# Optimization experiments

Hardware: AMD Instinct MI355X
Metric: run time of the kernel (lower is better)

## Reference

```python
import jax, jax.numpy as jnp
from jax import lax
import numpy as np


def conv2d(x, w, b, stride=1, pad=0):
    # x: [B,C,H,W], w: [O,I,kh,kw]
    y = lax.conv_general_dilated(
        x, w, (stride, stride), [(pad, pad), (pad, pad)],
        dimension_numbers=("NCHW", "OIHW", "NCHW"))
    return y + b[None, :, None, None]


def setup_inputs() -> dict:
    key = jax.random.key(0)
    ks = jax.random.split(key, 9)
    B, C, Ci, H, W = 1, 64, 32, 96, 96
    sc3 = 1.0 / np.sqrt(C * 9)   # fan-in scale for 3x3 convs
    sc1 = 1.0 / np.sqrt(C)       # fan-in scale for 1x1 convs
    scw = 1.0 / np.sqrt(Ci)
    return {
        "x":    jax.random.normal(ks[0], (B, C, H, W), jnp.float32),
        "d1_w": jax.random.normal(ks[1], (C, C, 3, 3), jnp.float32) * sc3,
        "d1_b": jnp.zeros((C,), jnp.float32),
        "d2_w": jax.random.normal(ks[2], (C, C, 3, 3), jnp.float32) * sc3,
        "d2_b": jnp.zeros((C,), jnp.float32),
        "d3_w": jax.random.normal(ks[3], (C, C, 3, 3), jnp.float32) * sc3,
        "d3_b": jnp.zeros((C,), jnp.float32),
        "g_w":  jax.random.normal(ks[4], (Ci, C, 1, 1), jnp.float32) * sc1,
        "g_b":  jnp.zeros((Ci,), jnp.float32),
        "th_w": jax.random.normal(ks[5], (Ci, C, 1, 1), jnp.float32) * sc1,
        "th_b": jnp.zeros((Ci,), jnp.float32),
        "ph_w": jax.random.normal(ks[6], (Ci, C, 1, 1), jnp.float32) * sc1,
        "ph_b": jnp.zeros((Ci,), jnp.float32),
        "W_w":  jax.random.normal(ks[7], (C, Ci, 1, 1), jnp.float32) * scw,
        "W_b":  jnp.zeros((C,), jnp.float32),
    }


def reference(x, d1_w, d1_b, d2_w, d2_b, d3_w, d3_b,
              g_w, g_b, th_w, th_b, ph_w, ph_b, W_w, W_b):
    lrelu = lambda v: jnp.where(v >= 0, v, 0.2 * v)
    y = lrelu(conv2d(x, d1_w, d1_b, stride=2, pad=1))
    y = lrelu(conv2d(y, d2_w, d2_b, stride=2, pad=1))
    y = conv2d(y, d3_w, d3_b, stride=2, pad=1)
    y = jax.image.resize(y, x.shape, method="bilinear")  # align_corners=False semantics
    x = jax.nn.sigmoid(y) * x
    # --- non-local block ---
    B, C, H, W = x.shape
    Ci = g_w.shape[0]
    gx = conv2d(x, g_w, g_b).reshape(B, Ci, -1)    # [B,Ci,N]
    tx = conv2d(x, th_w, th_b).reshape(B, Ci, -1)  # [B,Ci,N]
    px = conv2d(x, ph_w, ph_b).reshape(B, Ci, -1)  # [B,Ci,N]
    # f[b,n,m] = sum_c theta[b,n,c] * phi[b,c,m]  (N x N scores, no scaling)
    f = jnp.einsum("bcn,bcm->bnm", tx, px)
    f = jax.nn.softmax(f, axis=1)  # unconventional: softmax over FIRST token axis
    # y[b,c,n] = sum_m f[b,n,m] * g[b,c,m]
    y2 = jnp.einsum("bnm,bcm->bcn", f, gx).reshape(B, Ci, H, W)
    return conv2d(y2, W_w, W_b) + x
```

## Files before the change

### kernel.cpp

```cpp
#include <hip/hip_runtime.h>
#include <math.h>

#define NTOK 9216
#define CIN  32
#define CC   64
#define NCH1 24
#define NT1S 24
#define NCH2 16
#define MS2  18
#define MCH2 576
#define LOG2E 1.4426950408889634f
#define C1INIT (-17.312340490667560f)
#define C2INIT (-9.3123404906675595f)

typedef _Float16 half8 __attribute__((ext_vector_type(8)));
typedef _Float16 half4v __attribute__((ext_vector_type(4)));
typedef float    f32x4 __attribute__((ext_vector_type(4)));

static __device__ __forceinline__ float fexp2(float x) {
#if __has_builtin(__builtin_amdgcn_exp2f)
    return __builtin_amdgcn_exp2f(x);
#else
    return exp2f(x);
#endif
}

__global__ __launch_bounds__(192) void conv3x3_lds96(const float* __restrict__ in,
                                                     const float* __restrict__ w,
                                                     float* __restrict__ outp) {
    __shared__ float li[4][3][100];
    __shared__ float lw[4][9][64];
    const int t = threadIdx.x;
    const int oh = blockIdx.x, grp = blockIdx.y;
    const int ci0 = grp * 4;
    for (int idx = t; idx < 4 * 3 * 97; idx += 192) {
        int ci = idx / (3 * 97), rem = idx % (3 * 97);
        int kh = rem / 97, col = rem % 97;
        int ih = 2 * oh - 1 + kh, iw = col - 1;
        float v = 0.f;
        if (ih >= 0 && iw >= 0) v = in[(ci0 + ci) * 9216 + ih * 96 + iw];
        li[ci][kh][col] = v;
    }
    for (int idx = t; idx < 4 * 9 * 64; idx += 192) {
        int oc = idx / 36, r = idx % 36;
        int ci = r / 9, k = r % 9;
        lw[ci][k][oc] = w[oc * 576 + (ci0 + ci) * 9 + k];
    }
    __syncthreads();
    const int oc0 = (t & 15) * 4;
    const int ow0 = (t >> 4) * 4;
    float acc[4][4] = {};
    #pragma unroll
    for (int ci = 0; ci < 4; ++ci) {
        float wr[9][4];
        #pragma unroll
        for (int k = 0; k < 9; ++k)
            *(float4*)wr[k] = *(const float4*)&lw[ci][k][oc0];
        #pragma unroll
        for (int kh = 0; kh < 3; ++kh) {
            float v[9];
            #pragma unroll
            for (int j = 0; j < 9; ++j) v[j] = li[ci][kh][2 * ow0 + j];
            #pragma unroll
            for (int px = 0; px < 4; ++px)
                #pragma unroll
                for (int kw = 0; kw < 3; ++kw) {
                    float xv = v[2 * px + kw];
                    #pragma unroll
                    for (int o = 0; o < 4; ++o)
                        acc[px][o] = fmaf(xv, wr[kh * 3 + kw][o], acc[px][o]);
                }
        }
    }
    float* op = outp + grp * (CC * 2304) + oh * 48 + ow0;
    #pragma unroll
    for (int o = 0; o < 4; ++o)
        *(float4*)(op + (oc0 + o) * 2304) =
            make_float4(acc[0][o], acc[1][o], acc[2][o], acc[3][o]);
}

template<int HIN, int HOUT, int CIG>
__global__ void conv3x3_part(const float* __restrict__ in, const float* __restrict__ w,
                             float* __restrict__ outp) {
    const int p = blockIdx.x * blockDim.x + threadIdx.x;
    if (p >= HOUT * HOUT) return;
    const int oc = blockIdx.y, grp = blockIdx.z;
    const int oh = p / HOUT, ow = p % HOUT;
    const int ci0 = grp * CIG;
    float acc = 0.f;
    #pragma unroll
    for (int ci = 0; ci < CIG; ++ci) {
        const float* ip = in + (ci0 + ci) * HIN * HIN;
        const float* wp = w + oc * CC * 9 + (ci0 + ci) * 9;
        #pragma unroll
        for (int kh = 0; kh < 3; ++kh) {
            int ih = oh * 2 - 1 + kh;
            bool okh = (unsigned)ih < (unsigned)HIN;
            #pragma unroll
            for (int kw = 0; kw < 3; ++kw) {
                int iw = ow * 2 - 1 + kw;
                float v = (okh && (unsigned)iw < (unsigned)HIN) ? ip[ih * HIN + iw] : 0.f;
                acc = fmaf(v, wp[kh * 3 + kw], acc);
            }
        }
    }
    outp[grp * (CC * HOUT * HOUT) + oc * HOUT * HOUT + p] = acc;
}

template<int NG, int HW, int LRELU>
__global__ void conv_merge4(const float* __restrict__ parts, const float* __restrict__ b,
                            float* __restrict__ out) {
    int i4 = blockIdx.x * 256 + threadIdx.x;
    int oc = (i4 * 4) / HW;
    float bb = b[oc];
    float4 acc = make_float4(bb, bb, bb, bb);
    #pragma unroll
    for (int g = 0; g < NG; ++g) {
        float4 p = *(const float4*)(parts + g * (CC * HW) + i4 * 4);
        acc.x += p.x; acc.y += p.y; acc.z += p.z; acc.w += p.w;
    }
    if (LRELU) {
        acc.x = acc.x >= 0.f ? acc.x : 0.2f * acc.x;
        acc.y = acc.y >= 0.f ? acc.y : 0.2f * acc.y;
        acc.z = acc.z >= 0.f ? acc.z : 0.2f * acc.z;
        acc.w = acc.w >= 0.f ? acc.w : 0.2f * acc.w;
    }
    *(float4*)(out + i4 * 4) = acc;
}

static __device__ __forceinline__ float gate_val(const float* y3c, int n) {
    int h = n / 96, wc = n % 96;
    float fh = (h + 0.5f) * 0.125f - 0.5f;
    float fw = (wc + 0.5f) * 0.125f - 0.5f;
    int h0 = (int)floorf(fh); float ah = fh - (float)h0;
    int w0 = (int)floorf(fw); float aw = fw - (float)w0;
    int h0c = min(max(h0, 0), 11), h1c = min(max(h0 + 1, 0), 11);
    int w0c = min(max(w0, 0), 11), w1c = min(max(w0 + 1, 0), 11);
    float v = (1.f - ah) * ((1.f - aw) * y3c[h0c * 12 + w0c] + aw * y3c[h0c * 12 + w1c])
            +         ah * ((1.f - aw) * y3c[h1c * 12 + w0c] + aw * y3c[h1c * 12 + w1c]);
    return 1.f / (1.f + __expf(-v));
}

__global__ void gate_fused(const float* __restrict__ x, const float* __restrict__ cp3,
                           const float* __restrict__ d3b, float* __restrict__ xg) {
    __shared__ float y3c[144];
    const int b = blockIdx.x, t = threadIdx.x;
    const int c = b / 36;
    if (t < 144) {
        float acc = d3b[c];
        #pragma unroll
        for (int g = 0; g < 16; ++g)
            acc += cp3[g * (CC * 144) + c * 144 + t];
        y3c[t] = acc;
    }
    __syncthreads();
    int idx = b * 256 + t;
    int n = idx % 9216;
    float sg = gate_val(y3c, n);
    xg[idx] = sg * x[idx];
}

__global__ void conv1x1_frag(const float* __restrict__ xg,
                             const float* __restrict__ gw, const float* __restrict__ gb,
                             const float* __restrict__ thw, const float* __restrict__ thb,
                             const float* __restrict__ phw, const float* __restrict__ phb,
                             _Float16* __restrict__ txF, _Float16* __restrict__ pxF,
                             _Float16* __restrict__ gxF) {
    int ci = blockIdx.y;
    int n = blockIdx.x * 256 + threadIdx.x;
    float ag = gb[ci], at = thb[ci], ap = phb[ci];
    #pragma unroll 8
    for (int c = 0; c < CC; ++c) {
        float v = xg[c * NTOK + n];
        ag = fmaf(gw[ci * CC + c],  v, ag);
        at = fmaf(thw[ci * CC + c], v, at);
        ap = fmaf(phw[ci * CC + c], v, ap);
    }
    int addr_ab = (n >> 4) * 512 + (((n & 15) | (((ci & 15) >> 2) << 4)) * 8)
                + (((ci >> 4) << 2) | (ci & 3));
    txF[addr_ab] = (_Float16)(at * LOG2E);
    pxF[addr_ab] = (_Float16)ap;
    int addr_g = ((n >> 5) * 2 + (ci >> 4)) * 512
               + (((ci & 15) | (((n & 15) >> 2) << 4)) * 8)
               + ((((n >> 4) & 1) << 2) | (n & 3));
    gxF[addr_g] = (_Float16)ag;
}

__global__ __launch_bounds__(256) void phase1(const _Float16* __restrict__ txF,
                                              const _Float16* __restrict__ pxF,
                                              float* __restrict__ Dp) {
    int w = threadIdx.x >> 6, l = threadIdx.x & 63;
    int mtile0 = (blockIdx.x * 4 + w) * 4;
    half8 pf[4];
    #pragma unroll
    for (int j = 0; j < 4; ++j)
        pf[j] = *(const half8*)(pxF + (mtile0 + j) * 512 + l * 8);
    f32x4 cini = {C1INIT, C1INIT, C1INIT, C1INIT};
    float dsum[4][4] = {};
    int nt0 = blockIdx.y * NT1S;
    #pragma unroll 2
    for (int i = 0; i < NT1S; ++i) {
        half8 tf = *(const half8*)(txF + (nt0 + i) * 512 + l * 8);
        #pragma unroll
        for (int j = 0; j < 4; ++j) {
            f32x4 s = __builtin_amdgcn_mfma_f32_16x16x32_f16(pf[j], tf, cini, 0, 0, 0);
            #pragma unroll
            for (int r = 0; r < 4; ++r)
                dsum[j][r] += fexp2(s[r]);
        }
    }
    #pragma unroll
    for (int off = 1; off < 16; off <<= 1)
        #pragma unroll
        for (int j = 0; j < 4; ++j)
            #pragma unroll
            for (int r = 0; r < 4; ++r)
                dsum[j][r] += __shfl_xor(dsum[j][r], off);
    if ((l & 15) == 0) {
        #pragma unroll
        for (int j = 0; j < 4; ++j) {
            int m = (mtile0 + j) * 16 + (l >> 4) * 4;
            #pragma unroll
            for (int r = 0; r < 4; ++r)
                Dp[blockIdx.y * NTOK + m + r] = dsum[j][r];
        }
    }
}

__global__ __launch_bounds__(256) void phase2(const _Float16* __restrict__ txF,
                                              const _Float16* __restrict__ pxF,
                                              const _Float16* __restrict__ gxF,
                                              const float* __restrict__ Dp,
                                              _Float16* __restrict__ y2p) {
    __shared__ float l2D[MCH2];
    int mbase = blockIdx.y * MCH2;
    for (int i = threadIdx.x; i < MCH2; i += 256) {
        float D = 0.f;
        #pragma unroll
        for (int ch = 0; ch < NCH1; ++ch) D += Dp[ch * NTOK + mbase + i];
        l2D[i] = __log2f(D);
    }
    __syncthreads();
    int w = threadIdx.x >> 6, l = threadIdx.x & 63;
    int ntile0 = (blockIdx.x * 4 + w) * 4;
    half8 tf[4];
    #pragma unroll
    for (int j = 0; j < 4; ++j)
        tf[j] = *(const half8*)(txF + (ntile0 + j) * 512 + l * 8);
    int khi = (l >> 4) * 4;
    f32x4 zero = {0.f, 0.f, 0.f, 0.f};
    f32x4 c2v = {C2INIT, C2INIT, C2INIT, C2INIT};
    f32x4 acc[4][2];
    #pragma unroll
    for (int j = 0; j < 4; ++j) { acc[j][0] = zero; acc[j][1] = zero; }
    #pragma unroll 2
    for (int ms = 0; ms < MS2; ++ms) {
        int m0 = mbase + ms * 32;
        int mloc = ms * 32;
        int mt16 = m0 >> 4;
        half8 pf0 = *(const half8*)(pxF + mt16 * 512 + l * 8);
        half8 pf1 = *(const half8*)(pxF + (mt16 + 1) * 512 + l * 8);
        f32x4 l2a = *(const f32x4*)&l2D[mloc + khi];
        f32x4 l2b = *(const f32x4*)&l2D[mloc + 16 + khi];
        f32x4 cini0 = c2v - l2a;
        f32x4 cini1 = c2v - l2b;
        int gt = (m0 >> 5) * 2;
        half8 gf0 = *(const half8*)(gxF + gt * 512 + l * 8);
        half8 gf1 = *(const half8*)(gxF + (gt + 1) * 512 + l * 8);
        #pragma unroll
        for (int j = 0; j < 4; ++j) {
            f32x4 s0 = __builtin_amdgcn_mfma_f32_16x16x32_f16(pf0, tf[j], cini0, 0, 0, 0);
            f32x4 s1 = __builtin_amdgcn_mfma_f32_16x16x32_f16(pf1, tf[j], cini1, 0, 0, 0);
            half8 ff;
            #pragma unroll
            for (int r = 0; r < 4; ++r) {
                ff[r]     = (_Float16)fexp2(s0[r]);
                ff[4 + r] = (_Float16)fexp2(s1[r]);
            }
            acc[j][0] = __builtin_amdgcn_mfma_f32_16x16x32_f16(ff, gf0, acc[j][0], 0, 0, 0);
            acc[j][1] = __builtin_amdgcn_mfma_f32_16x16x32_f16(ff, gf1, acc[j][1], 0, 0, 0);
        }
    }
    _Float16* base = y2p + blockIdx.y * (CIN * NTOK);
    #pragma unroll
    for (int j = 0; j < 4; ++j) {
        int n = (ntile0 + j) * 16 + khi;
        half4v v0, v1;
        #pragma unroll
        for (int r = 0; r < 4; ++r) {
            v0[r] = (_Float16)(acc[j][0][r] * 0.00390625f);
            v1[r] = (_Float16)(acc[j][1][r] * 0.00390625f);
        }
        *(half4v*)(base + (l & 15) * NTOK + n)        = v0;
        *(half4v*)(base + (16 + (l & 15)) * NTOK + n) = v1;
    }
}

__global__ void mergeY2(const _Float16* __restrict__ y2p, float* __restrict__ att) {
    int i4 = blockIdx.x * 256 + threadIdx.x;
    float4 s = make_float4(0.f, 0.f, 0.f, 0.f);
    #pragma unroll
    for (int ch = 0; ch < NCH2; ++ch) {
        half4v p = *(const half4v*)(y2p + ch * (CIN * NTOK) + i4 * 4);
        s.x += (float)p[0]; s.y += (float)p[1]; s.z += (float)p[2]; s.w += (float)p[3];
    }
    *(float4*)(att + i4 * 4) = s;
}

__global__ void final_conv(const float* __restrict__ att, const float* __restrict__ Ww,
                           const float* __restrict__ Wb, const float* __restrict__ xg,
                           float* __restrict__ out) {
    int co = blockIdx.y;
    int n = blockIdx.x * 256 + threadIdx.x;
    float acc = Wb[co];
    #pragma unroll
    for (int ci = 0; ci < CIN; ++ci)
        acc = fmaf(Ww[co * CIN + ci], att[ci * NTOK + n], acc);
    out[co * NTOK + n] = acc + xg[co * NTOK + n];
}

extern "C" void kernel_launch(void* const* d_in, const int* in_sizes, int n_in,
                              void* d_out, int out_size, void* d_ws, size_t ws_size,
                              hipStream_t stream) {
    const float* x   = (const float*)d_in[0];
    const float* d1w = (const float*)d_in[1];  const float* d1b = (const float*)d_in[2];
    const float* d2w = (const float*)d_in[3];  const float* d2b = (const float*)d_in[4];
    const float* d3w = (const float*)d_in[5];  const float* d3b = (const float*)d_in[6];
    const float* gw  = (const float*)d_in[7];  const float* gb  = (const float*)d_in[8];
    const float* thw = (const float*)d_in[9];  const float* thb = (const float*)d_in[10];
    const float* phw = (const float*)d_in[11]; const float* phb = (const float*)d_in[12];
    const float* Ww  = (const float*)d_in[13]; const float* Wb  = (const float*)d_in[14];
    float* out = (float*)d_out;

    float* W    = (float*)d_ws;
    float* xg   = W;
    float* y1   = W + 589824;
    float* y2c  = W + 737280;
    float* Dp   = W + 774144;
    float* att  = W + 995328;
    float* cp1  = W + 1290240;
    float* cp2  = W + 3649536;
    float* cp3  = W + 4239360;
    _Float16* txF  = (_Float16*)(W + 4386816);
    _Float16* pxF  = (_Float16*)(W + 4534272);
    _Float16* gxF  = (_Float16*)(W + 4681728);
    _Float16* y2pH = (_Float16*)(W + 4829184);

    conv3x3_lds96<<<dim3(48, 16), 192, 0, stream>>>(x, d1w, cp1);
    conv_merge4<16, 2304, 1><<<144, 256, 0, stream>>>(cp1, d1b, y1);
    conv3x3_part<48, 24, 4><<<dim3(3, CC, 16), 192, 0, stream>>>(y1, d2w, cp2);
    conv_merge4<16, 576, 1><<<36, 256, 0, stream>>>(cp2, d2b, y2c);
    conv3x3_part<24, 12, 4><<<dim3(1, CC, 16), 192, 0, stream>>>(y2c, d3w, cp3);
    gate_fused<<<2304, 256, 0, stream>>>(x, cp3, d3b, xg);

    conv1x1_frag<<<dim3(36, CIN), 256, 0, stream>>>(xg, gw, gb, thw, thb, phw, phb,
                                                    txF, pxF, gxF);

    phase1<<<dim3(36, NCH1), 256, 0, stream>>>(txF, pxF, Dp);
    phase2<<<dim3(36, NCH2), 256, 0, stream>>>(txF, pxF, gxF, Dp, y2pH);
    mergeY2<<<288, 256, 0, stream>>>(y2pH, att);

    final_conv<<<dim3(36, CC), 256, 0, stream>>>(att, Ww, Wb, xg, out);
}
```

Baseline: 105.9 us.

## Stage shared operands in LDS across attention and conv kernels, widen conv1 channel groups

```diff
diff --git a/kernel.cpp b/kernel.cpp
--- a/kernel.cpp
+++ b/kernel.cpp
@@ -28,21 +28,21 @@
 __global__ __launch_bounds__(192) void conv3x3_lds96(const float* __restrict__ in,
                                                      const float* __restrict__ w,
                                                      float* __restrict__ outp) {
-    __shared__ float li[4][3][100];
-    __shared__ float lw[4][9][64];
+    __shared__ float li[8][3][100];
+    __shared__ float lw[8][9][64];
     const int t = threadIdx.x;
     const int oh = blockIdx.x, grp = blockIdx.y;
-    const int ci0 = grp * 4;
-    for (int idx = t; idx < 4 * 3 * 97; idx += 192) {
-        int ci = idx / (3 * 97), rem = idx % (3 * 97);
+    const int ci0 = grp * 8;
+    for (int idx = t; idx < 8 * 3 * 97; idx += 192) {
+        int ci = idx / 291, rem = idx % 291;
         int kh = rem / 97, col = rem % 97;
         int ih = 2 * oh - 1 + kh, iw = col - 1;
         float v = 0.f;
         if (ih >= 0 && iw >= 0) v = in[(ci0 + ci) * 9216 + ih * 96 + iw];
         li[ci][kh][col] = v;
     }
-    for (int idx = t; idx < 4 * 9 * 64; idx += 192) {
-        int oc = idx / 36, r = idx % 36;
+    for (int idx = t; idx < 8 * 9 * 64; idx += 192) {
+        int oc = idx / 72, r = idx % 72;
         int ci = r / 9, k = r % 9;
         lw[ci][k][oc] = w[oc * 576 + (ci0 + ci) * 9 + k];
     }
@@ -51,7 +51,7 @@
     const int ow0 = (t >> 4) * 4;
     float acc[4][4] = {};
     #pragma unroll
-    for (int ci = 0; ci < 4; ++ci) {
+    for (int ci = 0; ci < 8; ++ci) {
         float wr[9][4];
         #pragma unroll
         for (int k = 0; k < 9; ++k)
@@ -160,36 +160,59 @@
     xg[idx] = sg * x[idx];
 }
 
-__global__ void conv1x1_frag(const float* __restrict__ xg,
-                             const float* __restrict__ gw, const float* __restrict__ gb,
-                             const float* __restrict__ thw, const float* __restrict__ thb,
-                             const float* __restrict__ phw, const float* __restrict__ phb,
-                             _Float16* __restrict__ txF, _Float16* __restrict__ pxF,
-                             _Float16* __restrict__ gxF) {
-    int ci = blockIdx.y;
-    int n = blockIdx.x * 256 + threadIdx.x;
-    float ag = gb[ci], at = thb[ci], ap = phb[ci];
+__global__ __launch_bounds__(256) void conv1x1_frag(
+    const float* __restrict__ xg,
+    const float* __restrict__ gw, const float* __restrict__ gb,
+    const float* __restrict__ thw, const float* __restrict__ thb,
+    const float* __restrict__ phw, const float* __restrict__ phb,
+    _Float16* __restrict__ txF, _Float16* __restrict__ pxF,
+    _Float16* __restrict__ gxF) {
+    __shared__ float xgl[64][64];
+    const int t = threadIdx.x;
+    const int n0 = blockIdx.x * 64;
+    for (int idx = t; idx < 64 * 64; idx += 256) {
+        int c = idx >> 6, nl = idx & 63;
+        xgl[c][nl] = xg[c * NTOK + n0 + nl];
+    }
+    __syncthreads();
+    const int nl = t & 63, sub = t >> 6;
+    const int n = n0 + nl;
+    const int ci0 = blockIdx.y * 8 + sub * 2;
+    float ag[2], at[2], ap[2];
+    #pragma unroll
+    for (int j = 0; j < 2; ++j) {
+        ag[j] = gb[ci0 + j]; at[j] = thb[ci0 + j]; ap[j] = phb[ci0 + j];
+    }
     #pragma unroll 8
     for (int c = 0; c < CC; ++c) {
-        float v = xg[c * NTOK + n];
-        ag = fmaf(gw[ci * CC + c],  v, ag);
-        at = fmaf(thw[ci * CC + c], v, at);
-        ap = fmaf(phw[ci * CC + c], v, ap);
-    }
-    int addr_ab = (n >> 4) * 512 + (((n & 15) | (((ci & 15) >> 2) << 4)) * 8)
-                + (((ci >> 4) << 2) | (ci & 3));
-    txF[addr_ab] = (_Float16)(at * LOG2E);
-    pxF[addr_ab] = (_Float16)ap;
-    int addr_g = ((n >> 5) * 2 + (ci >> 4)) * 512
-               + (((ci & 15) | (((n & 15) >> 2) << 4)) * 8)
-               + ((((n >> 4) & 1) << 2) | (n & 3));
-    gxF[addr_g] = (_Float16)ag;
+        float v = xgl[c][nl];
+        #pragma unroll
+        for (int j = 0; j < 2; ++j) {
+            ag[j] = fmaf(gw[(ci0 + j) * CC + c],  v, ag[j]);
+            at[j] = fmaf(thw[(ci0 + j) * CC + c], v, at[j]);
+            ap[j] = fmaf(phw[(ci0 + j) * CC + c], v, ap[j]);
+        }
+    }
+    #pragma unroll
+    for (int j = 0; j < 2; ++j) {
+        int ci = ci0 + j;
+        int addr_ab = (n >> 4) * 512 + (((n & 15) | (((ci & 15) >> 2) << 4)) * 8)
+                    + (((ci >> 4) << 2) | (ci & 3));
+        txF[addr_ab] = (_Float16)(at[j] * LOG2E);
+        pxF[addr_ab] = (_Float16)ap[j];
+        int addr_g = ((n >> 5) * 2 + (ci >> 4)) * 512
+                   + (((ci & 15) | (((n & 15) >> 2) << 4)) * 8)
+                   + ((((n >> 4) & 1) << 2) | (n & 3));
+        gxF[addr_g] = (_Float16)ag[j];
+    }
 }
 
 __global__ __launch_bounds__(256) void phase1(const _Float16* __restrict__ txF,
                                               const _Float16* __restrict__ pxF,
                                               float* __restrict__ Dp) {
-    int w = threadIdx.x >> 6, l = threadIdx.x & 63;
+    __shared__ _Float16 tls[4][512];
+    const int t = threadIdx.x;
+    int w = t >> 6, l = t & 63;
     int mtile0 = (blockIdx.x * 4 + w) * 4;
     half8 pf[4];
     #pragma unroll
@@ -198,15 +221,22 @@
     f32x4 cini = {C1INIT, C1INIT, C1INIT, C1INIT};
     float dsum[4][4] = {};
     int nt0 = blockIdx.y * NT1S;
-    #pragma unroll 2
-    for (int i = 0; i < NT1S; ++i) {
-        half8 tf = *(const half8*)(txF + (nt0 + i) * 512 + l * 8);
-        #pragma unroll
-        for (int j = 0; j < 4; ++j) {
-            f32x4 s = __builtin_amdgcn_mfma_f32_16x16x32_f16(pf[j], tf, cini, 0, 0, 0);
-            #pragma unroll
-            for (int r = 0; r < 4; ++r)
-                dsum[j][r] += fexp2(s[r]);
+    const int ltile = t >> 6, loff = (t & 63) * 8;
+    for (int g = 0; g < NT1S / 4; ++g) {
+        __syncthreads();
+        *(half8*)(&tls[0][0] + t * 8) =
+            *(const half8*)(txF + (nt0 + g * 4 + ltile) * 512 + loff);
+        __syncthreads();
+        #pragma unroll
+        for (int i = 0; i < 4; ++i) {
+            half8 tf = *(const half8*)(&tls[i][l * 8]);
+            #pragma unroll
+            for (int j = 0; j < 4; ++j) {
+                f32x4 s = __builtin_amdgcn_mfma_f32_16x16x32_f16(pf[j], tf, cini, 0, 0, 0);
+                #pragma unroll
+                for (int r = 0; r < 4; ++r)
+                    dsum[j][r] += fexp2(s[r]);
+            }
         }
     }
     #pragma unroll
@@ -233,15 +263,16 @@
                                               const float* __restrict__ Dp,
                                               _Float16* __restrict__ y2p) {
     __shared__ float l2D[MCH2];
+    __shared__ _Float16 pg[8][512];
+    const int t = threadIdx.x;
     int mbase = blockIdx.y * MCH2;
-    for (int i = threadIdx.x; i < MCH2; i += 256) {
+    for (int i = t; i < MCH2; i += 256) {
         float D = 0.f;
         #pragma unroll
         for (int ch = 0; ch < NCH1; ++ch) D += Dp[ch * NTOK + mbase + i];
         l2D[i] = __log2f(D);
     }
-    __syncthreads();
-    int w = threadIdx.x >> 6, l = threadIdx.x & 63;
+    int w = t >> 6, l = t & 63;
     int ntile0 = (blockIdx.x * 4 + w) * 4;
     half8 tf[4];
     #pragma unroll
@@ -253,32 +284,42 @@
     f32x4 acc[4][2];
     #pragma unroll
     for (int j = 0; j < 4; ++j) { acc[j][0] = zero; acc[j][1] = zero; }
-    #pragma unroll 2
-    for (int ms = 0; ms < MS2; ++ms) {
-        int m0 = mbase + ms * 32;
-        int mloc = ms * 32;
-        int mt16 = m0 >> 4;
-        half8 pf0 = *(const half8*)(pxF + mt16 * 512 + l * 8);
-        half8 pf1 = *(const half8*)(pxF + (mt16 + 1) * 512 + l * 8);
-        f32x4 l2a = *(const f32x4*)&l2D[mloc + khi];
-        f32x4 l2b = *(const f32x4*)&l2D[mloc + 16 + khi];
-        f32x4 cini0 = c2v - l2a;
-        f32x4 cini1 = c2v - l2b;
-        int gt = (m0 >> 5) * 2;
-        half8 gf0 = *(const half8*)(gxF + gt * 512 + l * 8);
-        half8 gf1 = *(const half8*)(gxF + (gt + 1) * 512 + l * 8);
-        #pragma unroll
-        for (int j = 0; j < 4; ++j) {
-            f32x4 s0 = __builtin_amdgcn_mfma_f32_16x16x32_f16(pf0, tf[j], cini0, 0, 0, 0);
-            f32x4 s1 = __builtin_amdgcn_mfma_f32_16x16x32_f16(pf1, tf[j], cini1, 0, 0, 0);
-            half8 ff;
-            #pragma unroll
-            for (int r = 0; r < 4; ++r) {
-                ff[r]     = (_Float16)fexp2(s0[r]);
-                ff[4 + r] = (_Float16)fexp2(s1[r]);
+    for (int g = 0; g < MS2 / 2; ++g) {
+        int pb = (mbase + g * 64) >> 4;
+        __syncthreads();
+        #pragma unroll
+        for (int uu = 0; uu < 2; ++uu) {
+            int u = t + uu * 256;
+            int tile = u >> 6, off = (u & 63) * 8;
+            const _Float16* s = (tile < 4) ? (pxF + (pb + tile) * 512 + off)
+                                           : (gxF + (pb + tile - 4) * 512 + off);
+            *(half8*)(&pg[0][0] + u * 8) = *(const half8*)s;
+        }
+        __syncthreads();
+        #pragma unroll
+        for (int s2 = 0; s2 < 2; ++s2) {
+            int mloc = g * 64 + s2 * 32;
+            half8 pf0 = *(const half8*)(&pg[2 * s2][l * 8]);
+            half8 pf1 = *(const half8*)(&pg[2 * s2 + 1][l * 8]);
+            half8 gf0 = *(const half8*)(&pg[4 + 2 * s2][l * 8]);
+            half8 gf1 = *(const half8*)(&pg[5 + 2 * s2][l * 8]);
+            f32x4 l2a = *(const f32x4*)&l2D[mloc + khi];
+            f32x4 l2b = *(const f32x4*)&l2D[mloc + 16 + khi];
+            f32x4 cini0 = c2v - l2a;
+            f32x4 cini1 = c2v - l2b;
+            #pragma unroll
+            for (int j = 0; j < 4; ++j) {
+                f32x4 s0 = __builtin_amdgcn_mfma_f32_16x16x32_f16(pf0, tf[j], cini0, 0, 0, 0);
+                f32x4 s1 = __builtin_amdgcn_mfma_f32_16x16x32_f16(pf1, tf[j], cini1, 0, 0, 0);
+                half8 ff;
+                #pragma unroll
+                for (int r = 0; r < 4; ++r) {
+                    ff[r]     = (_Float16)fexp2(s0[r]);
+                    ff[4 + r] = (_Float16)fexp2(s1[r]);
+                }
+                acc[j][0] = __builtin_amdgcn_mfma_f32_16x16x32_f16(ff, gf0, acc[j][0], 0, 0, 0);
+                acc[j][1] = __builtin_amdgcn_mfma_f32_16x16x32_f16(ff, gf1, acc[j][1], 0, 0, 0);
             }
-            acc[j][0] = __builtin_amdgcn_mfma_f32_16x16x32_f16(ff, gf0, acc[j][0], 0, 0, 0);
-            acc[j][1] = __builtin_amdgcn_mfma_f32_16x16x32_f16(ff, gf1, acc[j][1], 0, 0, 0);
         }
     }
     _Float16* base = y2p + blockIdx.y * (CIN * NTOK);
@@ -339,22 +380,22 @@
     float* Dp   = W + 774144;
     float* att  = W + 995328;
     float* cp1  = W + 1290240;
-    float* cp2  = W + 3649536;
-    float* cp3  = W + 4239360;
-    _Float16* txF  = (_Float16*)(W + 4386816);
-    _Float16* pxF  = (_Float16*)(W + 4534272);
-    _Float16* gxF  = (_Float16*)(W + 4681728);
-    _Float16* y2pH = (_Float16*)(W + 4829184);
-
-    conv3x3_lds96<<<dim3(48, 16), 192, 0, stream>>>(x, d1w, cp1);
-    conv_merge4<16, 2304, 1><<<144, 256, 0, stream>>>(cp1, d1b, y1);
+    float* cp2  = W + 2469888;
+    float* cp3  = W + 3059712;
+    _Float16* txF  = (_Float16*)(W + 3207168);
+    _Float16* pxF  = (_Float16*)(W + 3354624);
+    _Float16* gxF  = (_Float16*)(W + 3502080);
+    _Float16* y2pH = (_Float16*)(W + 3649536);
+
+    conv3x3_lds96<<<dim3(48, 8), 192, 0, stream>>>(x, d1w, cp1);
+    conv_merge4<8, 2304, 1><<<144, 256, 0, stream>>>(cp1, d1b, y1);
     conv3x3_part<48, 24, 4><<<dim3(3, CC, 16), 192, 0, stream>>>(y1, d2w, cp2);
     conv_merge4<16, 576, 1><<<36, 256, 0, stream>>>(cp2, d2b, y2c);
     conv3x3_part<24, 12, 4><<<dim3(1, CC, 16), 192, 0, stream>>>(y2c, d3w, cp3);
     gate_fused<<<2304, 256, 0, stream>>>(x, cp3, d3b, xg);
 
-    conv1x1_frag<<<dim3(36, CIN), 256, 0, stream>>>(xg, gw, gb, thw, thb, phw, phb,
-                                                    txF, pxF, gxF);
+    conv1x1_frag<<<dim3(144, 4), 256, 0, stream>>>(xg, gw, gb, thw, thb, phw, phb,
+                                                   txF, pxF, gxF);
 
     phase1<<<dim3(36, NCH1), 256, 0, stream>>>(txF, pxF, Dp);
     phase2<<<dim3(36, NCH2), 256, 0, stream>>>(txF, pxF, gxF, Dp, y2pH);
```

Result: slower. 116.8 us (+10.3%).
